# Kernel tuning notes

Hardware: AMD Instinct MI355X
Metric: run time of the kernel (lower is better)

The kernel has to match this reference:

```python
import jax, jax.numpy as jnp
import numpy as np

H = 64
VOCAB = 64
READ_FREQ = 16


def setup_inputs() -> dict:
    key = jax.random.key(0)
    ks = jax.random.split(key, 16)
    B, L, M = 512, 2048, 256
    seq = jax.random.randint(ks[0], (B, L), 0, VOCAB)
    memory = jax.random.normal(ks[1], (B, M, H), dtype=jnp.float32)
    s = 0.1
    return {
        "seq": seq,
        "memory": memory,
        "embed_w": jax.random.normal(ks[2], (VOCAB, H), jnp.float32) * s,
        "gru_w_ih": jax.random.normal(ks[3], (3 * H, 2 * H), jnp.float32) * s,
        "gru_w_hh": jax.random.normal(ks[4], (3 * H, H), jnp.float32) * s,
        "gru_b_ih": jax.random.normal(ks[5], (3 * H,), jnp.float32) * s,
        "gru_b_hh": jax.random.normal(ks[6], (3 * H,), jnp.float32) * s,
        "key_w": jax.random.normal(ks[7], (H, H), jnp.float32) * s,
        "key_b": jax.random.normal(ks[8], (H,), jnp.float32) * s,
        "val_w": jax.random.normal(ks[9], (H, H), jnp.float32) * s,
        "val_b": jax.random.normal(ks[10], (H,), jnp.float32) * s,
        "query_w": jax.random.normal(ks[11], (H, H), jnp.float32) * s,
        "query_b": jax.random.normal(ks[12], (H,), jnp.float32) * s,
        "head_w": jax.random.normal(ks[13], (VOCAB, H), jnp.float32) * s,
        "head_b": jax.random.normal(ks[14], (VOCAB,), jnp.float32) * s,
    }


def _forward(seq, memory, embed_w, gru_w_ih, gru_w_hh, gru_b_ih, gru_b_hh,
             key_w, key_b, val_w, val_b, query_w, query_b, head_w, head_b):
    B, L = seq.shape
    scale = 1.0 / (H ** 0.5)
    # memory is fixed: precompute keys/values once (B, M, H)
    k = jnp.einsum("bmh,kh->bmk", memory, key_w) + key_b
    v = jnp.einsum("bmh,kh->bmk", memory, val_w) + val_b
    # embed all tokens up front: (B, L, H) -> chunks (C, F, B, H)
    emb = embed_w[seq]
    C = L // READ_FREQ
    emb_chunks = emb.reshape(B, C, READ_FREQ, H).transpose(1, 2, 0, 3)

    def gru_step(carry, x_t):
        h, retrieved = carry
        inp = jnp.concatenate([x_t, retrieved], axis=-1)  # (B, 2H)
        gi = inp @ gru_w_ih.T + gru_b_ih                   # (B, 3H)
        gh = h @ gru_w_hh.T + gru_b_hh                     # (B, 3H)
        i_r, i_z, i_n = jnp.split(gi, 3, axis=-1)
        h_r, h_z, h_n = jnp.split(gh, 3, axis=-1)
        r = jax.nn.sigmoid(i_r + h_r)
        z = jax.nn.sigmoid(i_z + h_z)
        n = jnp.tanh(i_n + r * h_n)
        h_new = (1.0 - z) * n + z * h
        return (h_new, retrieved), None

    def chunk_step(h, chunk_emb):  # chunk_emb: (READ_FREQ, B, H)
        q = h @ query_w.T + query_b                        # (B, H)
        scores = jnp.einsum("bh,bmh->bm", q, k) * scale
        w = jax.nn.softmax(scores, axis=-1)
        retrieved = jnp.einsum("bm,bmh->bh", w, v)
        (h, _), _ = jax.lax.scan(gru_step, (h, retrieved), chunk_emb)
        return h, None

    h0 = jnp.zeros((B, H), dtype=memory.dtype)
    h, _ = jax.lax.scan(chunk_step, h0, emb_chunks)
    return h @ head_w.T + head_b                            # (B, VOCAB)


def reference(seq, memory, embed_w, gru_w_ih, gru_w_hh, gru_b_ih, gru_b_hh,
              key_w, key_b, val_w, val_b, query_w, query_b, head_w, head_b):
    return _forward(seq, memory, embed_w, gru_w_ih, gru_w_hh, gru_b_ih, gru_b_hh,
                    key_w, key_b, val_w, val_b, query_w, query_b, head_w, head_b)
```

## Files before the change

### kernel.cpp

```cpp
#include <hip/hip_runtime.h>
#include <hip/hip_fp16.h>


#define B_ 512
#define L_ 2048
#define M_ 256
#define H_ 64
#define C_ 128
#define F_ 16

typedef float v2f __attribute__((ext_vector_type(2)));
typedef _Float16 h2v __attribute__((ext_vector_type(2)));

#if __has_builtin(__builtin_amdgcn_fdot2)
__device__ __forceinline__ float FDOT2(h2v a, h2v b, float c) {
    return __builtin_amdgcn_fdot2(a, b, c, false);
}
#else
__device__ __forceinline__ float FDOT2(h2v a, h2v b, float c) {
    return c + (float)a[0]*(float)b[0] + (float)a[1]*(float)b[1];
}
#endif

__device__ __forceinline__ h2v bch(unsigned u) { return __builtin_bit_cast(h2v, u); }
__device__ __forceinline__ unsigned rl_u(unsigned v, int lane) {
    return (unsigned)__builtin_amdgcn_readlane((int)v, lane);
}
__device__ __forceinline__ float rl(float v, int lane) {
    return __int_as_float(__builtin_amdgcn_readlane(__float_as_int(v), lane));
}
__device__ __forceinline__ unsigned pkrtz(float a, float b) {
    auto r = __builtin_amdgcn_cvt_pkrtz(a, b);
    return __builtin_bit_cast(unsigned, r);
}
__device__ __forceinline__ float dot4(float4 a, float4 b) {
    return a.x*b.x + a.y*b.y + a.z*b.z + a.w*b.w;
}
__device__ __forceinline__ float fast_rcp(float x) { return __builtin_amdgcn_rcpf(x); }
__device__ __forceinline__ float sigm(float x) { return fast_rcp(1.f + __expf(-x)); }
__device__ __forceinline__ float tanh_f(float x) {
    float e2 = __expf(-2.f * fabsf(x));
    return copysignf((1.f - e2) * fast_rcp(1.f + e2), x);
}
__device__ __forceinline__ unsigned h2rn(float a, float b) {
    __half2 h = __floats2half2_rn(a, b);
    return __builtin_bit_cast(unsigned, h);
}

#define WS_KT    0u
#define WS_V     16777216u
#define WS_G4    33554432u
#define WS_WPHH  33619968u
#define WS_WR    33644544u
#define WS_KQP   33669120u
#define WS_VWP   33685504u
#define WS_KQF   33701888u
#define WS_BQ    33718272u
#define WS_KQV   33718528u
#define WS_C0    33718784u
#define WS_CB    33719040u

#define S_KT   0u
#define S_V    32768u
#define SMEM_BYTES 66560u

__global__ void pack_weights(const float* __restrict__ w_ih,
                             const float* __restrict__ w_hh,
                             const float* __restrict__ vw,
                             unsigned* __restrict__ WPhh2,
                             unsigned* __restrict__ WR2p,
                             float4* __restrict__ VWP)
{
    int idx = blockIdx.x * 256 + threadIdx.x;
    if (idx < 6144) {
        int j = idx & 63, t = idx >> 6, g = t % 3, k2 = t / 3;
        const float* s = w_hh + (g*64 + j)*64 + 2*k2;
        WPhh2[idx] = h2rn(s[0], s[1]);
    } else if (idx < 12288) {
        int i = idx - 6144;
        int j = i & 63, t = i >> 6, g = t % 3, k2 = t / 3;
        const float* s = w_ih + (g*64 + j)*128 + 64 + 2*k2;
        WR2p[i] = h2rn(s[0], s[1]);
    } else if (idx < 13312) {
        int i = idx - 12288;
        int j = i & 63, k4 = i >> 6;
        const float* s = vw + j*64 + 4*k4;
        VWP[i] = make_float4(s[0], s[1], s[2], s[3]);
    }
}

__global__ __launch_bounds__(64) void fold_kq(const float* __restrict__ kw,
                                              const float* __restrict__ qw,
                                              const float* __restrict__ kb,
                                              const float* __restrict__ qb,
                                              float* __restrict__ KQf,
                                              float* __restrict__ bqv,
                                              float* __restrict__ kqv,
                                              float* __restrict__ c0p)
{
    int d = blockIdx.x, j = threadIdx.x;
    __shared__ float kcol[64], kbs[64], qbs[64];
    kcol[j] = kw[j*64 + d];
    kbs[j]  = kb[j];
    qbs[j]  = qb[j];
    __syncthreads();
    float acc = 0.f, accq = 0.f;
    for (int t = 0; t < 64; ++t) {
        float kc = kcol[t];
        acc  += kc * qw[t*64 + j];
        accq += kc * qbs[t];
    }
    KQf[d*64 + j] = acc;
    if (j == 0) kqv[d] = accq;
    if (d == 0) {
        float vb = 0.f;
        for (int t = 0; t < 64; ++t) vb += kbs[t] * qw[t*64 + j];
        bqv[j] = vb;
        if (j == 0) {
            float c0 = 0.f;
            for (int t = 0; t < 64; ++t) c0 += kbs[t] * qbs[t];
            *c0p = c0;
        }
    }
}

__global__ __launch_bounds__(256) void pack_kq(const float* __restrict__ KQf,
                                               float4* __restrict__ KQP)
{
    int i = blockIdx.x * 256 + threadIdx.x;
    if (i < 1024) {
        int o = i & 63, k4 = i >> 6;
        KQP[i] = make_float4(KQf[(4*k4+0)*64 + o], KQf[(4*k4+1)*64 + o],
                             KQf[(4*k4+2)*64 + o], KQf[(4*k4+3)*64 + o]);
    }
}

__global__ __launch_bounds__(64) void build_G(const float* __restrict__ embed_w,
                                              const float* __restrict__ w_ih,
                                              const float* __restrict__ b_ih,
                                              float4* __restrict__ G4)
{
    int v = blockIdx.x, j = threadIdx.x;
    __shared__ float e_s[64];
    e_s[j] = embed_w[v*64 + j];
    __syncthreads();
    float a0 = b_ih[j], a1 = b_ih[64 + j], a2 = b_ih[128 + j];
    for (int k = 0; k < 64; ++k) {
        float e = e_s[k];
        a0 += e * w_ih[j*128 + k];
        a1 += e * w_ih[(64 + j)*128 + k];
        a2 += e * w_ih[(128 + j)*128 + k];
    }
    G4[v*64 + j] = make_float4(a0, a1, a2, 0.f);
}

__global__ __launch_bounds__(256) void compute_kv(const float* __restrict__ memory,
                                                  const float* __restrict__ bqv,
                                                  const float* __restrict__ val_b,
                                                  const float4* __restrict__ KQP,
                                                  const float4* __restrict__ VWP,
                                                  const float* __restrict__ kqv,
                                                  const float* __restrict__ c0p,
                                                  unsigned* __restrict__ kT2,
                                                  unsigned* __restrict__ vT2,
                                                  float* __restrict__ cB)
{
    int wid = threadIdx.x >> 6;
    int o   = threadIdx.x & 63;
    int row = blockIdx.x * 4 + wid;
    int b = row >> 8, m = row & 255;
    __shared__ __align__(16) float mem_s[4][64];
    __shared__ float avs[4][64];
    mem_s[wid][o] = memory[(size_t)row * 64 + o];
    __syncthreads();
    float ak = bqv[o], av = val_b[o], ac = *c0p;
    const float4* m4  = (const float4*)mem_s[wid];
    const float4* kq4 = (const float4*)kqv;
#pragma unroll
    for (int k4 = 0; k4 < 16; ++k4) {
        float4 mm = m4[k4];
        ak += dot4(mm, KQP[k4*64 + o]);
        av += dot4(mm, VWP[k4*64 + o]);
        ac += dot4(mm, kq4[k4]);
    }
    float nb = __shfl_xor(ak, 1);
    if ((o & 1) == 0)
        kT2[((size_t)b*32 + (o >> 1))*256 + m] = h2rn(ak, nb);
    avs[wid][o] = av;
    if (o == 0) cB[row] = ac;
    __syncthreads();
    if ((wid & 1) == 0) {
        vT2[((size_t)b*64 + o)*128 + (m >> 1)] = h2rn(avs[wid][o], avs[wid+1][o]);
    }
}

#define GRU_STEP(cg0, cg1, cg2) do {                                        \
    float gr = RrB, gz = RzB, gn = bhn;                                     \
    _Pragma("unroll")                                                       \
    for (int kp = 0; kp < 32; ++kp) {                                       \
        h2v hhp = bch(rl_u(hpu, 2*kp));                                     \
        gr = FDOT2(hhp, wr2[kp], gr);                                       \
        gz = FDOT2(hhp, wz2[kp], gz);                                       \
        gn = FDOT2(hhp, wn2[kp], gn);                                       \
    }                                                                       \
    float r_ = sigm(gr + (cg0));                                            \
    float z_ = sigm(gz + (cg1));                                            \
    float n_ = tanh_f(((cg2) + Rn) + r_ * gn);                              \
    h = fmaf(z_, h - n_, n_);                                               \
    float hx_ = __shfl_xor(h, 1);                                           \
    hpu = pkrtz(h, hx_);                                                    \
} while (0)

__global__ __launch_bounds__(64, 1) void recurrent_main(
    const int*   __restrict__ seq,
    const float* __restrict__ b_hh,
    const float* __restrict__ head_w,
    const float* __restrict__ head_b,
    const unsigned* __restrict__ kT2g,
    const unsigned* __restrict__ vT2g,
    const float4* __restrict__ G4,
    const unsigned* __restrict__ WPhh2,
    const unsigned* __restrict__ WR2p,
    const float* __restrict__ cB,
    float* __restrict__ out)
{
    const int b = blockIdx.x;
    const int j = threadIdx.x;

    extern __shared__ __align__(16) char smem[];
    const uint4* kT2_lds = (const uint4*)(smem + S_KT);

    {
        const uint4* kTg = (const uint4*)(kT2g + (size_t)b * 8192);
        uint4* kTls = (uint4*)(smem + S_KT);
#pragma unroll
        for (int i = 0; i < 32; ++i) kTls[i*64 + j] = kTg[i*64 + j];
        const uint4* vg4 = (const uint4*)(vT2g + (size_t)b * 8192);
        uint4* vls4 = (uint4*)(smem + S_V);
#pragma unroll
        for (int i = 0; i < 32; ++i) {
            int t = i*64 + j;
            vls4[(t >> 5)*33 + (t & 31)] = vg4[t];
        }
    }

    h2v wr2[32], wz2[32], wn2[32];
#pragma unroll
    for (int k2 = 0; k2 < 32; ++k2) {
        wr2[k2] = bch(WPhh2[(k2*3 + 0)*64 + j]);
        wz2[k2] = bch(WPhh2[(k2*3 + 1)*64 + j]);
        wn2[k2] = bch(WPhh2[(k2*3 + 2)*64 + j]);
    }
    h2v rr2[32], rz2[32], rn2[32];
#pragma unroll
    for (int k2 = 0; k2 < 32; ++k2) {
        rr2[k2] = bch(WR2p[(k2*3 + 0)*64 + j]);
        rz2[k2] = bch(WR2p[(k2*3 + 1)*64 + j]);
        rn2[k2] = bch(WR2p[(k2*3 + 2)*64 + j]);
    }

    float h = 0.f;
    unsigned hpu = 0u;
    const float bhr = b_hh[j], bhz = b_hh[64 + j], bhn = b_hh[128 + j];
    const float4 cc = *(const float4*)(cB + (size_t)b*256 + 4*j);

    const int* seqb = seq + (size_t)b * L_;
    const uint4* vrow = (const uint4*)(smem + S_V) + j*33;
    __builtin_amdgcn_wave_barrier();

    for (int c = 0; c < C_; ++c) {
        const int c16 = c * F_;

        const int4 qA = *(const int4*)(seqb + c16);
        const int4 qB = *(const int4*)(seqb + c16 + 4);
        const int4 qC = *(const int4*)(seqb + c16 + 8);
        const int4 qD = *(const int4*)(seqb + c16 + 12);
        const int tA0 = __builtin_amdgcn_readfirstlane(qA.x);
        const int tA1 = __builtin_amdgcn_readfirstlane(qA.y);
        const int tA2 = __builtin_amdgcn_readfirstlane(qA.z);
        const int tA3 = __builtin_amdgcn_readfirstlane(qA.w);
        const int tB0 = __builtin_amdgcn_readfirstlane(qB.x);
        const int tB1 = __builtin_amdgcn_readfirstlane(qB.y);
        const int tB2 = __builtin_amdgcn_readfirstlane(qB.z);
        const int tB3 = __builtin_amdgcn_readfirstlane(qB.w);
        const int tC0 = __builtin_amdgcn_readfirstlane(qC.x);
        const int tC1 = __builtin_amdgcn_readfirstlane(qC.y);
        const int tC2 = __builtin_amdgcn_readfirstlane(qC.z);
        const int tC3 = __builtin_amdgcn_readfirstlane(qC.w);
        const int tD0 = __builtin_amdgcn_readfirstlane(qD.x);
        const int tD1 = __builtin_amdgcn_readfirstlane(qD.y);
        const int tD2 = __builtin_amdgcn_readfirstlane(qD.z);
        const int tD3 = __builtin_amdgcn_readfirstlane(qD.w);

        float s0 = cc.x, s1 = cc.y, s2 = cc.z, s3 = cc.w;
#pragma unroll 8
        for (int t = 0; t < 32; ++t) {
            h2v qq = bch(rl_u(hpu, 2*t));
            uint4 kk = kT2_lds[t*64 + j];
            s0 = FDOT2(bch(kk.x), qq, s0);
            s1 = FDOT2(bch(kk.y), qq, s1);
            s2 = FDOT2(bch(kk.z), qq, s2);
            s3 = FDOT2(bch(kk.w), qq, s3);
        }
        const float scale = 0.125f;
        float4 p;
        p.x = __expf(s0*scale); p.y = __expf(s1*scale);
        p.z = __expf(s2*scale); p.w = __expf(s3*scale);
        const unsigned ppu0 = pkrtz(p.x, p.y);
        const unsigned ppu1 = pkrtz(p.z, p.w);
        float sum = (p.x + p.y) + (p.z + p.w);
#pragma unroll
        for (int o = 32; o > 0; o >>= 1) sum += __shfl_xor(sum, o);
        float inv = fast_rcp(sum);

        float r0 = 0.f, r1 = 0.f, r2 = 0.f, r3 = 0.f;
#pragma unroll 8
        for (int qd = 0; qd < 32; ++qd) {
            uint4 vv = vrow[qd];
            unsigned px = rl_u(ppu0, 2*qd);
            unsigned py = rl_u(ppu1, 2*qd);
            unsigned pz = rl_u(ppu0, 2*qd + 1);
            unsigned pw = rl_u(ppu1, 2*qd + 1);
            r0 = FDOT2(bch(px), bch(vv.x), r0);
            r1 = FDOT2(bch(py), bch(vv.y), r1);
            r2 = FDOT2(bch(pz), bch(vv.z), r2);
            r3 = FDOT2(bch(pw), bch(vv.w), r3);
        }
        float ret = ((r0 + r1) + (r2 + r3)) * inv;

        float rx = __shfl_xor(ret, 1);
        unsigned rpu = pkrtz(ret, rx);
        float Rr = 0.f, Rz = 0.f, Rn = 0.f;
#pragma unroll
        for (int k2 = 0; k2 < 32; ++k2) {
            h2v rr = bch(rl_u(rpu, 2*k2));
            Rr = FDOT2(rr, rr2[k2], Rr);
            Rz = FDOT2(rr, rz2[k2], Rz);
            Rn = FDOT2(rr, rn2[k2], Rn);
        }
        const float RrB = Rr + bhr, RzB = Rz + bhz;

#pragma unroll 1
        for (int g = 0; g < 4; ++g) {
            const bool gb1 = (g & 1), gb2 = (g & 2);
            const int t0 = gb2 ? (gb1 ? tD0 : tC0) : (gb1 ? tB0 : tA0);
            const int t1 = gb2 ? (gb1 ? tD1 : tC1) : (gb1 ? tB1 : tA1);
            const int t2 = gb2 ? (gb1 ? tD2 : tC2) : (gb1 ? tB2 : tA2);
            const int t3 = gb2 ? (gb1 ? tD3 : tC3) : (gb1 ? tB3 : tA3);
            const float4 gA = G4[t0*64 + j];
            const float4 gB = G4[t1*64 + j];
            const float4 gC = G4[t2*64 + j];
            const float4 gD = G4[t3*64 + j];

            GRU_STEP(gA.x, gA.y, gA.z);
            GRU_STEP(gB.x, gB.y, gB.z);
            GRU_STEP(gC.x, gC.y, gC.z);
            GRU_STEP(gD.x, gD.y, gD.z);
        }
    }

    float o = head_b[j];
#pragma unroll
    for (int k4 = 0; k4 < 16; ++k4) {
        float h0 = rl(h, 4*k4+0), h1 = rl(h, 4*k4+1);
        float h2 = rl(h, 4*k4+2), h3 = rl(h, 4*k4+3);
        const float* hw = head_w + j*64 + 4*k4;
        o += h0*hw[0] + h1*hw[1] + h2*hw[2] + h3*hw[3];
    }
    out[(size_t)b*64 + j] = o;
}

extern "C" void kernel_launch(void* const* d_in, const int* in_sizes, int n_in,
                              void* d_out, int out_size, void* d_ws, size_t ws_size,
                              hipStream_t stream) {
    const int*   seq      = (const int*)  d_in[0];
    const float* memory   = (const float*)d_in[1];
    const float* embed_w  = (const float*)d_in[2];
    const float* w_ih     = (const float*)d_in[3];
    const float* w_hh     = (const float*)d_in[4];
    const float* b_ih     = (const float*)d_in[5];
    const float* b_hh     = (const float*)d_in[6];
    const float* key_w    = (const float*)d_in[7];
    const float* key_b    = (const float*)d_in[8];
    const float* val_w    = (const float*)d_in[9];
    const float* val_b    = (const float*)d_in[10];
    const float* query_w  = (const float*)d_in[11];
    const float* query_b  = (const float*)d_in[12];
    const float* head_w   = (const float*)d_in[13];
    const float* head_b   = (const float*)d_in[14];

    char* ws = (char*)d_ws;
    unsigned* kT2  = (unsigned*)(ws + WS_KT);
    unsigned* vT2  = (unsigned*)(ws + WS_V);
    float4*   G4   = (float4*)  (ws + WS_G4);
    unsigned* WPhh2 = (unsigned*)(ws + WS_WPHH);
    unsigned* WR2p  = (unsigned*)(ws + WS_WR);
    float4*   KQP   = (float4*)  (ws + WS_KQP);
    float4*   VWP   = (float4*)  (ws + WS_VWP);
    float*    KQf   = (float*)   (ws + WS_KQF);
    float*    bqv   = (float*)   (ws + WS_BQ);
    float*    kqv   = (float*)   (ws + WS_KQV);
    float*    c0p   = (float*)   (ws + WS_C0);
    float*    cB    = (float*)   (ws + WS_CB);

    (void)hipFuncSetAttribute((const void*)recurrent_main,
                              hipFuncAttributeMaxDynamicSharedMemorySize,
                              (int)SMEM_BYTES);

    pack_weights<<<64, 256, 0, stream>>>(w_ih, w_hh, val_w, WPhh2, WR2p, VWP);
    fold_kq<<<64, 64, 0, stream>>>(key_w, query_w, key_b, query_b,
                                   KQf, bqv, kqv, c0p);
    pack_kq<<<4, 256, 0, stream>>>(KQf, KQP);
    build_G<<<64, 64, 0, stream>>>(embed_w, w_ih, b_ih, G4);
    compute_kv<<<(B_*M_)/4, 256, 0, stream>>>(memory, bqv, val_b, KQP, VWP,
                                              kqv, c0p, kT2, vT2, cB);
    recurrent_main<<<B_, 64, SMEM_BYTES, stream>>>(seq, b_hh, head_w, head_b,
                                                   kT2, vT2, G4, WPhh2, WR2p, cB,
                                                   (float*)d_out);
}
```

Measured before the change: 1.268 ms.

## Process two batch rows per wavefront to interleave independent GRU recurrences

Each 64-thread block now handles two batch elements, running both sequential recurrences interleaved so their independent dot-product chains can hide each other's latency and share register-resident weights. Shared memory doubles to hold keys and values for both rows, and the grid is halved to 256 blocks. The cost is fewer blocks than CUs on MI355X, more registers and LDS per block, and twice the instruction work per wave, so the gain depends on whether the single-row version was latency-bound.

Measured after the change: 2.127 ms. 67.8% more time.

```diff
diff --git a/kernel.cpp b/kernel.cpp
--- a/kernel.cpp
+++ b/kernel.cpp
@@ -60,9 +60,11 @@
 #define WS_C0    33718784u
 #define WS_CB    33719040u
 
-#define S_KT   0u
-#define S_V    32768u
-#define SMEM_BYTES 66560u
+#define S_KT0  0u
+#define S_KT1  32768u
+#define S_V0   65536u
+#define S_V1   99328u
+#define SMEM_BYTES 133120u
 
 __global__ void pack_weights(const float* __restrict__ w_ih,
                              const float* __restrict__ w_hh,
@@ -194,21 +196,30 @@
     }
 }
 
-#define GRU_STEP(cg0, cg1, cg2) do {                                        \
-    float gr = RrB, gz = RzB, gn = bhn;                                     \
+#define GRU_STEP2(cA0, cA1, cA2, cB0, cB1, cB2) do {                        \
+    float gr0 = RrB0, gz0 = RzB0, gn0 = bhn;                                \
+    float gr1 = RrB1, gz1 = RzB1, gn1 = bhn;                                \
     _Pragma("unroll")                                                       \
     for (int kp = 0; kp < 32; ++kp) {                                       \
-        h2v hhp = bch(rl_u(hpu, 2*kp));                                     \
-        gr = FDOT2(hhp, wr2[kp], gr);                                       \
-        gz = FDOT2(hhp, wz2[kp], gz);                                       \
-        gn = FDOT2(hhp, wn2[kp], gn);                                       \
+        h2v ha = bch(rl_u(hpu0, 2*kp));                                     \
+        h2v hb = bch(rl_u(hpu1, 2*kp));                                     \
+        gr0 = FDOT2(ha, wr2[kp], gr0);                                      \
+        gr1 = FDOT2(hb, wr2[kp], gr1);                                      \
+        gz0 = FDOT2(ha, wz2[kp], gz0);                                      \
+        gz1 = FDOT2(hb, wz2[kp], gz1);                                      \
+        gn0 = FDOT2(ha, wn2[kp], gn0);                                      \
+        gn1 = FDOT2(hb, wn2[kp], gn1);                                      \
     }                                                                       \
-    float r_ = sigm(gr + (cg0));                                            \
-    float z_ = sigm(gz + (cg1));                                            \
-    float n_ = tanh_f(((cg2) + Rn) + r_ * gn);                              \
-    h = fmaf(z_, h - n_, n_);                                               \
-    float hx_ = __shfl_xor(h, 1);                                           \
-    hpu = pkrtz(h, hx_);                                                    \
+    float r_0 = sigm(gr0 + (cA0));                                          \
+    float r_1 = sigm(gr1 + (cB0));                                          \
+    float z_0 = sigm(gz0 + (cA1));                                          \
+    float z_1 = sigm(gz1 + (cB1));                                          \
+    float n_0 = tanh_f(((cA2) + Rn0) + r_0 * gn0);                          \
+    float n_1 = tanh_f(((cB2) + Rn1) + r_1 * gn1);                          \
+    h0 = fmaf(z_0, h0 - n_0, n_0);                                          \
+    h1 = fmaf(z_1, h1 - n_1, n_1);                                          \
+    hpu0 = pkrtz(h0, __shfl_xor(h0, 1));                                    \
+    hpu1 = pkrtz(h1, __shfl_xor(h1, 1));                                    \
 } while (0)
 
 __global__ __launch_bounds__(64, 1) void recurrent_main(
@@ -224,23 +235,33 @@
     const float* __restrict__ cB,
     float* __restrict__ out)
 {
-    const int b = blockIdx.x;
+    const int b0 = blockIdx.x * 2;
+    const int b1 = b0 + 1;
     const int j = threadIdx.x;
 
     extern __shared__ __align__(16) char smem[];
-    const uint4* kT2_lds = (const uint4*)(smem + S_KT);
+    const uint4* kT0_lds = (const uint4*)(smem + S_KT0);
+    const uint4* kT1_lds = (const uint4*)(smem + S_KT1);
 
     {
-        const uint4* kTg = (const uint4*)(kT2g + (size_t)b * 8192);
-        uint4* kTls = (uint4*)(smem + S_KT);
-#pragma unroll
-        for (int i = 0; i < 32; ++i) kTls[i*64 + j] = kTg[i*64 + j];
-        const uint4* vg4 = (const uint4*)(vT2g + (size_t)b * 8192);
-        uint4* vls4 = (uint4*)(smem + S_V);
+        const uint4* kTg0 = (const uint4*)(kT2g + (size_t)b0 * 8192);
+        const uint4* kTg1 = (const uint4*)(kT2g + (size_t)b1 * 8192);
+        uint4* kTls0 = (uint4*)(smem + S_KT0);
+        uint4* kTls1 = (uint4*)(smem + S_KT1);
+#pragma unroll
+        for (int i = 0; i < 32; ++i) {
+            kTls0[i*64 + j] = kTg0[i*64 + j];
+            kTls1[i*64 + j] = kTg1[i*64 + j];
+        }
+        const uint4* vg0 = (const uint4*)(vT2g + (size_t)b0 * 8192);
+        const uint4* vg1 = (const uint4*)(vT2g + (size_t)b1 * 8192);
+        uint4* vls0 = (uint4*)(smem + S_V0);
+        uint4* vls1 = (uint4*)(smem + S_V1);
 #pragma unroll
         for (int i = 0; i < 32; ++i) {
             int t = i*64 + j;
-            vls4[(t >> 5)*33 + (t & 31)] = vg4[t];
+            vls0[(t >> 5)*33 + (t & 31)] = vg0[t];
+            vls1[(t >> 5)*33 + (t & 31)] = vg1[t];
         }
     }
 
@@ -259,22 +280,29 @@
         rn2[k2] = bch(WR2p[(k2*3 + 2)*64 + j]);
     }
 
-    float h = 0.f;
-    unsigned hpu = 0u;
+    float h0 = 0.f, h1 = 0.f;
+    unsigned hpu0 = 0u, hpu1 = 0u;
     const float bhr = b_hh[j], bhz = b_hh[64 + j], bhn = b_hh[128 + j];
-    const float4 cc = *(const float4*)(cB + (size_t)b*256 + 4*j);
-
-    const int* seqb = seq + (size_t)b * L_;
-    const uint4* vrow = (const uint4*)(smem + S_V) + j*33;
+    const float4 cc0 = *(const float4*)(cB + (size_t)b0*256 + 4*j);
+    const float4 cc1 = *(const float4*)(cB + (size_t)b1*256 + 4*j);
+
+    const int* seqb0 = seq + (size_t)b0 * L_;
+    const int* seqb1 = seq + (size_t)b1 * L_;
+    const uint4* vrow0 = (const uint4*)(smem + S_V0) + j*33;
+    const uint4* vrow1 = (const uint4*)(smem + S_V1) + j*33;
     __builtin_amdgcn_wave_barrier();
 
     for (int c = 0; c < C_; ++c) {
         const int c16 = c * F_;
 
-        const int4 qA = *(const int4*)(seqb + c16);
-        const int4 qB = *(const int4*)(seqb + c16 + 4);
-        const int4 qC = *(const int4*)(seqb + c16 + 8);
-        const int4 qD = *(const int4*)(seqb + c16 + 12);
+        const int4 qA = *(const int4*)(seqb0 + c16);
+        const int4 qB = *(const int4*)(seqb0 + c16 + 4);
+        const int4 qC = *(const int4*)(seqb0 + c16 + 8);
+        const int4 qD = *(const int4*)(seqb0 + c16 + 12);
+        const int4 wA = *(const int4*)(seqb1 + c16);
+        const int4 wB = *(const int4*)(seqb1 + c16 + 4);
+        const int4 wC = *(const int4*)(seqb1 + c16 + 8);
+        const int4 wD = *(const int4*)(seqb1 + c16 + 12);
         const int tA0 = __builtin_amdgcn_readfirstlane(qA.x);
         const int tA1 = __builtin_amdgcn_readfirstlane(qA.y);
         const int tA2 = __builtin_amdgcn_readfirstlane(qA.z);
@@ -291,83 +319,140 @@
         const int tD1 = __builtin_amdgcn_readfirstlane(qD.y);
         const int tD2 = __builtin_amdgcn_readfirstlane(qD.z);
         const int tD3 = __builtin_amdgcn_readfirstlane(qD.w);
-
-        float s0 = cc.x, s1 = cc.y, s2 = cc.z, s3 = cc.w;
+        const int uA0 = __builtin_amdgcn_readfirstlane(wA.x);
+        const int uA1 = __builtin_amdgcn_readfirstlane(wA.y);
+        const int uA2 = __builtin_amdgcn_readfirstlane(wA.z);
+        const int uA3 = __builtin_amdgcn_readfirstlane(wA.w);
+        const int uB0 = __builtin_amdgcn_readfirstlane(wB.x);
+        const int uB1 = __builtin_amdgcn_readfirstlane(wB.y);
+        const int uB2 = __builtin_amdgcn_readfirstlane(wB.z);
+        const int uB3 = __builtin_amdgcn_readfirstlane(wB.w);
+        const int uC0 = __builtin_amdgcn_readfirstlane(wC.x);
+        const int uC1 = __builtin_amdgcn_readfirstlane(wC.y);
+        const int uC2 = __builtin_amdgcn_readfirstlane(wC.z);
+        const int uC3 = __builtin_amdgcn_readfirstlane(wC.w);
+        const int uD0 = __builtin_amdgcn_readfirstlane(wD.x);
+        const int uD1 = __builtin_amdgcn_readfirstlane(wD.y);
+        const int uD2 = __builtin_amdgcn_readfirstlane(wD.z);
+        const int uD3 = __builtin_amdgcn_readfirstlane(wD.w);
+
+        float s00 = cc0.x, s01 = cc0.y, s02 = cc0.z, s03 = cc0.w;
+        float s10 = cc1.x, s11 = cc1.y, s12 = cc1.z, s13 = cc1.w;
 #pragma unroll 8
         for (int t = 0; t < 32; ++t) {
-            h2v qq = bch(rl_u(hpu, 2*t));
-            uint4 kk = kT2_lds[t*64 + j];
-            s0 = FDOT2(bch(kk.x), qq, s0);
-            s1 = FDOT2(bch(kk.y), qq, s1);
-            s2 = FDOT2(bch(kk.z), qq, s2);
-            s3 = FDOT2(bch(kk.w), qq, s3);
+            h2v qq0 = bch(rl_u(hpu0, 2*t));
+            h2v qq1 = bch(rl_u(hpu1, 2*t));
+            uint4 k0 = kT0_lds[t*64 + j];
+            uint4 k1 = kT1_lds[t*64 + j];
+            s00 = FDOT2(bch(k0.x), qq0, s00);
+            s10 = FDOT2(bch(k1.x), qq1, s10);
+            s01 = FDOT2(bch(k0.y), qq0, s01);
+            s11 = FDOT2(bch(k1.y), qq1, s11);
+            s02 = FDOT2(bch(k0.z), qq0, s02);
+            s12 = FDOT2(bch(k1.z), qq1, s12);
+            s03 = FDOT2(bch(k0.w), qq0, s03);
+            s13 = FDOT2(bch(k1.w), qq1, s13);
         }
         const float scale = 0.125f;
-        float4 p;
-        p.x = __expf(s0*scale); p.y = __expf(s1*scale);
-        p.z = __expf(s2*scale); p.w = __expf(s3*scale);
-        const unsigned ppu0 = pkrtz(p.x, p.y);
-        const unsigned ppu1 = pkrtz(p.z, p.w);
-        float sum = (p.x + p.y) + (p.z + p.w);
-#pragma unroll
-        for (int o = 32; o > 0; o >>= 1) sum += __shfl_xor(sum, o);
-        float inv = fast_rcp(sum);
-
-        float r0 = 0.f, r1 = 0.f, r2 = 0.f, r3 = 0.f;
+        float4 p0, p1;
+        p0.x = __expf(s00*scale); p0.y = __expf(s01*scale);
+        p0.z = __expf(s02*scale); p0.w = __expf(s03*scale);
+        p1.x = __expf(s10*scale); p1.y = __expf(s11*scale);
+        p1.z = __expf(s12*scale); p1.w = __expf(s13*scale);
+        const unsigned pp00 = pkrtz(p0.x, p0.y);
+        const unsigned pp01 = pkrtz(p0.z, p0.w);
+        const unsigned pp10 = pkrtz(p1.x, p1.y);
+        const unsigned pp11 = pkrtz(p1.z, p1.w);
+        float sum0 = (p0.x + p0.y) + (p0.z + p0.w);
+        float sum1 = (p1.x + p1.y) + (p1.z + p1.w);
+#pragma unroll
+        for (int o = 32; o > 0; o >>= 1) {
+            sum0 += __shfl_xor(sum0, o);
+            sum1 += __shfl_xor(sum1, o);
+        }
+        float inv0 = fast_rcp(sum0);
+        float inv1 = fast_rcp(sum1);
+
+        float r00 = 0.f, r01 = 0.f, r02 = 0.f, r03 = 0.f;
+        float r10 = 0.f, r11 = 0.f, r12 = 0.f, r13 = 0.f;
 #pragma unroll 8
         for (int qd = 0; qd < 32; ++qd) {
-            uint4 vv = vrow[qd];
-            unsigned px = rl_u(ppu0, 2*qd);
-            unsigned py = rl_u(ppu1, 2*qd);
-            unsigned pz = rl_u(ppu0, 2*qd + 1);
-            unsigned pw = rl_u(ppu1, 2*qd + 1);
-            r0 = FDOT2(bch(px), bch(vv.x), r0);
-            r1 = FDOT2(bch(py), bch(vv.y), r1);
-            r2 = FDOT2(bch(pz), bch(vv.z), r2);
-            r3 = FDOT2(bch(pw), bch(vv.w), r3);
-        }
-        float ret = ((r0 + r1) + (r2 + r3)) * inv;
-
-        float rx = __shfl_xor(ret, 1);
-        unsigned rpu = pkrtz(ret, rx);
-        float Rr = 0.f, Rz = 0.f, Rn = 0.f;
+            uint4 v0 = vrow0[qd];
+            uint4 v1 = vrow1[qd];
+            unsigned px0 = rl_u(pp00, 2*qd);
+            unsigned px1 = rl_u(pp10, 2*qd);
+            unsigned py0 = rl_u(pp01, 2*qd);
+            unsigned py1 = rl_u(pp11, 2*qd);
+            unsigned pz0 = rl_u(pp00, 2*qd + 1);
+            unsigned pz1 = rl_u(pp10, 2*qd + 1);
+            unsigned pw0 = rl_u(pp01, 2*qd + 1);
+            unsigned pw1 = rl_u(pp11, 2*qd + 1);
+            r00 = FDOT2(bch(px0), bch(v0.x), r00);
+            r10 = FDOT2(bch(px1), bch(v1.x), r10);
+            r01 = FDOT2(bch(py0), bch(v0.y), r01);
+            r11 = FDOT2(bch(py1), bch(v1.y), r11);
+            r02 = FDOT2(bch(pz0), bch(v0.z), r02);
+            r12 = FDOT2(bch(pz1), bch(v1.z), r12);
+            r03 = FDOT2(bch(pw0), bch(v0.w), r03);
+            r13 = FDOT2(bch(pw1), bch(v1.w), r13);
+        }
+        float ret0 = ((r00 + r01) + (r02 + r03)) * inv0;
+        float ret1 = ((r10 + r11) + (r12 + r13)) * inv1;
+
+        unsigned rpu0 = pkrtz(ret0, __shfl_xor(ret0, 1));
+        unsigned rpu1 = pkrtz(ret1, __shfl_xor(ret1, 1));
+        float Rr0 = 0.f, Rz0 = 0.f, Rn0 = 0.f;
+        float Rr1 = 0.f, Rz1 = 0.f, Rn1 = 0.f;
 #pragma unroll
         for (int k2 = 0; k2 < 32; ++k2) {
-            h2v rr = bch(rl_u(rpu, 2*k2));
-            Rr = FDOT2(rr, rr2[k2], Rr);
-            Rz = FDOT2(rr, rz2[k2], Rz);
-            Rn = FDOT2(rr, rn2[k2], Rn);
-        }
-        const float RrB = Rr + bhr, RzB = Rz + bhz;
+            h2v ra = bch(rl_u(rpu0, 2*k2));
+            h2v rb = bch(rl_u(rpu1, 2*k2));
+            Rr0 = FDOT2(ra, rr2[k2], Rr0);
+            Rr1 = FDOT2(rb, rr2[k2], Rr1);
+            Rz0 = FDOT2(ra, rz2[k2], Rz0);
+            Rz1 = FDOT2(rb, rz2[k2], Rz1);
+            Rn0 = FDOT2(ra, rn2[k2], Rn0);
+            Rn1 = FDOT2(rb, rn2[k2], Rn1);
+        }
+        const float RrB0 = Rr0 + bhr, RzB0 = Rz0 + bhz;
+        const float RrB1 = Rr1 + bhr, RzB1 = Rz1 + bhz;
 
 #pragma unroll 1
         for (int g = 0; g < 4; ++g) {
             const bool gb1 = (g & 1), gb2 = (g & 2);
-            const int t0 = gb2 ? (gb1 ? tD0 : tC0) : (gb1 ? tB0 : tA0);
-            const int t1 = gb2 ? (gb1 ? tD1 : tC1) : (gb1 ? tB1 : tA1);
-            const int t2 = gb2 ? (gb1 ? tD2 : tC2) : (gb1 ? tB2 : tA2);
-            const int t3 = gb2 ? (gb1 ? tD3 : tC3) : (gb1 ? tB3 : tA3);
-            const float4 gA = G4[t0*64 + j];
-            const float4 gB = G4[t1*64 + j];
-            const float4 gC = G4[t2*64 + j];
-            const float4 gD = G4[t3*64 + j];
-
-            GRU_STEP(gA.x, gA.y, gA.z);
-            GRU_STEP(gB.x, gB.y, gB.z);
-            GRU_STEP(gC.x, gC.y, gC.z);
-            GRU_STEP(gD.x, gD.y, gD.z);
-        }
-    }
-
-    float o = head_b[j];
+            const int x0 = gb2 ? (gb1 ? tD0 : tC0) : (gb1 ? tB0 : tA0);
+            const int x1 = gb2 ? (gb1 ? tD1 : tC1) : (gb1 ? tB1 : tA1);
+            const int x2 = gb2 ? (gb1 ? tD2 : tC2) : (gb1 ? tB2 : tA2);
+            const int x3 = gb2 ? (gb1 ? tD3 : tC3) : (gb1 ? tB3 : tA3);
+            const int y0 = gb2 ? (gb1 ? uD0 : uC0) : (gb1 ? uB0 : uA0);
+            const int y1 = gb2 ? (gb1 ? uD1 : uC1) : (gb1 ? uB1 : uA1);
+            const int y2 = gb2 ? (gb1 ? uD2 : uC2) : (gb1 ? uB2 : uA2);
+            const int y3 = gb2 ? (gb1 ? uD3 : uC3) : (gb1 ? uB3 : uA3);
+            const float4 fA0 = G4[x0*64 + j], fA1 = G4[y0*64 + j];
+            const float4 fB0 = G4[x1*64 + j], fB1 = G4[y1*64 + j];
+            const float4 fC0 = G4[x2*64 + j], fC1 = G4[y2*64 + j];
+            const float4 fD0 = G4[x3*64 + j], fD1 = G4[y3*64 + j];
+
+            GRU_STEP2(fA0.x, fA0.y, fA0.z, fA1.x, fA1.y, fA1.z);
+            GRU_STEP2(fB0.x, fB0.y, fB0.z, fB1.x, fB1.y, fB1.z);
+            GRU_STEP2(fC0.x, fC0.y, fC0.z, fC1.x, fC1.y, fC1.z);
+            GRU_STEP2(fD0.x, fD0.y, fD0.z, fD1.x, fD1.y, fD1.z);
+        }
+    }
+
+    float o0 = head_b[j], o1 = o0;
 #pragma unroll
     for (int k4 = 0; k4 < 16; ++k4) {
-        float h0 = rl(h, 4*k4+0), h1 = rl(h, 4*k4+1);
-        float h2 = rl(h, 4*k4+2), h3 = rl(h, 4*k4+3);
         const float* hw = head_w + j*64 + 4*k4;
-        o += h0*hw[0] + h1*hw[1] + h2*hw[2] + h3*hw[3];
-    }
-    out[(size_t)b*64 + j] = o;
+        float a0 = rl(h0, 4*k4+0), a1 = rl(h0, 4*k4+1);
+        float a2 = rl(h0, 4*k4+2), a3 = rl(h0, 4*k4+3);
+        float b0v = rl(h1, 4*k4+0), b1v = rl(h1, 4*k4+1);
+        float b2v = rl(h1, 4*k4+2), b3v = rl(h1, 4*k4+3);
+        o0 += a0*hw[0] + a1*hw[1] + a2*hw[2] + a3*hw[3];
+        o1 += b0v*hw[0] + b1v*hw[1] + b2v*hw[2] + b3v*hw[3];
+    }
+    out[(size_t)b0*64 + j] = o0;
+    out[(size_t)b1*64 + j] = o1;
 }
 
 extern "C" void kernel_launch(void* const* d_in, const int* in_sizes, int n_in,
@@ -414,7 +499,7 @@
     build_G<<<64, 64, 0, stream>>>(embed_w, w_ih, b_ih, G4);
     compute_kv<<<(B_*M_)/4, 256, 0, stream>>>(memory, bqv, val_b, KQP, VWP,
                                               kqv, c0p, kT2, vT2, cB);
-    recurrent_main<<<B_, 64, SMEM_BYTES, stream>>>(seq, b_hh, head_w, head_b,
-                                                   kT2, vT2, G4, WPhh2, WR2p, cB,
-                                                   (float*)d_out);
-}
+    recurrent_main<<<B_/2, 64, SMEM_BYTES, stream>>>(seq, b_hh, head_w, head_b,
+                                                     kT2, vT2, G4, WPhh2, WR2p, cB,
+                                                     (float*)d_out);
+}
```
